# Kernel tuning notes

Hardware: AMD Instinct MI355X
Metric: run time of the kernel (lower is better)

The kernel has to match this reference:

```python
import jax, jax.numpy as jnp
import numpy as np

N = 50000
E = 800000
D = 128          # in_channels == hidden_channels
L = 3            # num_layers
JK = D * L       # jk 'cat' output
H2 = D // 2      # classifier hidden
C = 2            # out classes
EPS = 1e-5


def setup_inputs() -> dict:
    key = jax.random.key(0)
    ks = jax.random.split(key, 16)
    x = jax.random.normal(ks[0], (N, D), dtype=jnp.float32)
    edge_index = jax.random.randint(ks[1], (2, E), 0, N, dtype=jnp.int64)
    s = 0.05
    Wl = jax.random.normal(ks[2], (L, D, D), dtype=jnp.float32) * s   # lin_l (on aggregated), has bias
    bl = jax.random.normal(ks[3], (L, D), dtype=jnp.float32) * s
    Wr = jax.random.normal(ks[4], (L, D, D), dtype=jnp.float32) * s   # lin_r (on root), no bias
    gamma = jnp.ones((L, D), dtype=jnp.float32)
    beta = jnp.zeros((L, D), dtype=jnp.float32)
    rmean = jax.random.normal(ks[5], (L, D), dtype=jnp.float32) * s
    rvar = jax.random.uniform(ks[6], (L, D), dtype=jnp.float32, minval=0.5, maxval=1.5)
    Wc1 = jax.random.normal(ks[7], (JK, H2), dtype=jnp.float32) * s
    bc1 = jax.random.normal(ks[8], (H2,), dtype=jnp.float32) * s
    Wc2 = jax.random.normal(ks[9], (H2, C), dtype=jnp.float32) * s
    bc2 = jax.random.normal(ks[10], (C,), dtype=jnp.float32) * s
    return {"x": x, "edge_index": edge_index, "Wl": Wl, "bl": bl, "Wr": Wr,
            "gamma": gamma, "beta": beta, "rmean": rmean, "rvar": rvar,
            "Wc1": Wc1, "bc1": bc1, "Wc2": Wc2, "bc2": bc2}


def reference(x, edge_index, Wl, bl, Wr, gamma, beta, rmean, rvar, Wc1, bc1, Wc2, bc2):
    src, dst = edge_index[0], edge_index[1]
    # node in-degree (for mean aggregation), clamp to avoid div-by-zero
    deg = jax.ops.segment_sum(jnp.ones((E,), dtype=x.dtype), dst, num_segments=N)
    inv_deg = 1.0 / jnp.maximum(deg, 1.0)  # [N]

    h = x
    layer_outputs = []
    for i in range(L):
        # SAGEConv(mean): out = lin_l(mean_{j in N(i)} h_j) + lin_r(h_i)
        agg = jax.ops.segment_sum(h[src], dst, num_segments=N) * inv_deg[:, None]  # [N, D]
        h = agg @ Wl[i] + bl[i] + h @ Wr[i]
        # BatchNorm (eval: running stats), then ReLU; Dropout is identity in eval
        h = (h - rmean[i]) * jax.lax.rsqrt(rvar[i] + EPS) * gamma[i] + beta[i]
        h = jax.nn.relu(h)
        layer_outputs.append(h)

    jk = jnp.concatenate(layer_outputs, axis=-1)  # [N, L*D]
    z = jax.nn.relu(jk @ Wc1 + bc1)
    logits = z @ Wc2 + bc2  # [N, 2]
    return logits
```

## Files before the change

kernel.cpp:

```cpp
#include <hip/hip_runtime.h>
#include <hip/hip_fp16.h>
#include <cstdint>
#include <cstddef>

#define DD 128
#define JKD 384
#define EPSV 1e-5f
#define BSH 7
#define NBMAX 512
#define PCH 8192
#define PTH 1024
#define BCAP 8192

typedef __attribute__((ext_vector_type(8))) short bf16x8;
typedef __attribute__((ext_vector_type(4))) float f32x4;
#define MFMA(a, b, c) __builtin_amdgcn_mfma_f32_16x16x32_bf16(a, b, c, 0, 0, 0)

__device__ inline unsigned short f2bf_rne(float f) {
  unsigned u = __float_as_uint(f);
  unsigned r = u + 0x7fffu + ((u >> 16) & 1u);
  return (unsigned short)(r >> 16);
}

__device__ inline void split8(const float* s, bf16x8& hi, bf16x8& lo) {
#pragma unroll
  for (int j = 0; j < 8; ++j) {
    float f = s[j];
    unsigned short h = f2bf_rne(f);
    float fh = __uint_as_float((unsigned)h << 16);
    hi[j] = (short)h;
    lo[j] = (short)f2bf_rne(f - fh);
  }
}

__device__ inline void h8_to_f8(uint4 raw, float* out) {
  const __half2* hp = reinterpret_cast<const __half2*>(&raw);
#pragma unroll
  for (int j = 0; j < 4; ++j) {
    float2 f = __half22float2(hp[j]);
    out[2 * j] = f.x;
    out[2 * j + 1] = f.y;
  }
}

__global__ __launch_bounds__(PTH) void bucket_hist(const int* __restrict__ dst,
                                                   int* __restrict__ hist_g, int E) {
  __shared__ int h[NBMAX];
  int t = threadIdx.x;
  for (int i = t; i < NBMAX; i += PTH) h[i] = 0;
  __syncthreads();
  int base = blockIdx.x * PCH;
#pragma unroll
  for (int it = 0; it < PCH / PTH; ++it) {
    int e = base + it * PTH + t;
    if (e < E) {
      int d = __builtin_nontemporal_load(dst + e);
      atomicAdd(&h[d >> BSH], 1);
    }
  }
  __syncthreads();
  for (int i = t; i < NBMAX; i += PTH) hist_g[blockIdx.x * NBMAX + i] = h[i];
}

__global__ __launch_bounds__(512) void bucket_scan(const int* __restrict__ hist_g, int nChunks,
                                                   int* __restrict__ bucket_start,
                                                   int* __restrict__ bucket_cursor,
                                                   int* __restrict__ row_start, int N, int E) {
  __shared__ int wsum[8];
  __shared__ int wpref[8];
  int t = threadIdx.x;
  int lane = t & 63, wid = t >> 6;
  int v = 0;
  for (int c = 0; c < nChunks; ++c) v += hist_g[c * NBMAX + t];
  int sc = v;
#pragma unroll
  for (int off = 1; off < 64; off <<= 1) {
    int u = __shfl_up(sc, off, 64);
    if (lane >= off) sc += u;
  }
  if (lane == 63) wsum[wid] = sc;
  __syncthreads();
  if (t == 0) {
    int a = 0;
#pragma unroll
    for (int w = 0; w < 8; ++w) { wpref[w] = a; a += wsum[w]; }
  }
  __syncthreads();
  int excl = wpref[wid] + sc - v;
  bucket_start[t] = excl;
  bucket_cursor[t] = excl;
  if (t == 0) row_start[N] = E;
}

__global__ __launch_bounds__(PTH) void partition_prep(
    const int* __restrict__ src, const int* __restrict__ dst, int* bucket_cursor,
    unsigned* __restrict__ packed, int E, int nChunks,
    const float* __restrict__ Wl, const float* __restrict__ Wr, bf16x8* __restrict__ wf,
    const float* __restrict__ Wc1, bf16x8* __restrict__ wcf,
    const float* __restrict__ x, unsigned short* __restrict__ x16, int N) {
  __shared__ int h[NBMAX];
  __shared__ int lofs[NBMAX];
  __shared__ int res[NBMAX];
  __shared__ int lcur[NBMAX];
  __shared__ int wsum[4];
  __shared__ int wpref[4];
  __shared__ unsigned stage[PCH];

  if (blockIdx.x < nChunks) {
    int t = threadIdx.x;
    int lane = t & 63;
    int base = blockIdx.x * PCH;
    for (int i = t; i < NBMAX; i += PTH) h[i] = 0;
    __syncthreads();
#pragma unroll
    for (int it = 0; it < PCH / PTH; ++it) {
      int e = base + it * PTH + t;
      if (e < E) {
        int d = __builtin_nontemporal_load(dst + e);
        atomicAdd(&h[d >> BSH], 1);
      }
    }
    __syncthreads();
    int c0 = 0, c1 = 0, s = 0, sc = 0;
    if (t < 256) {
      c0 = h[2 * t];
      c1 = h[2 * t + 1];
      s = c0 + c1;
      sc = s;
#pragma unroll
      for (int off = 1; off < 64; off <<= 1) {
        int u = __shfl_up(sc, off, 64);
        if (lane >= off) sc += u;
      }
      if (lane == 63) wsum[t >> 6] = sc;
    }
    __syncthreads();
    if (t == 0) {
      int a = 0;
#pragma unroll
      for (int w = 0; w < 4; ++w) { wpref[w] = a; a += wsum[w]; }
    }
    __syncthreads();
    if (t < 256) {
      int excl = wpref[t >> 6] + sc - s;
      lofs[2 * t] = excl;
      lofs[2 * t + 1] = excl + c0;
      lcur[2 * t] = excl;
      lcur[2 * t + 1] = excl + c0;
      if (c0 > 0) res[2 * t] = atomicAdd(&bucket_cursor[2 * t], c0);
      if (c1 > 0) res[2 * t + 1] = atomicAdd(&bucket_cursor[2 * t + 1], c1);
    }
    __syncthreads();
#pragma unroll
    for (int it = 0; it < PCH / PTH; ++it) {
      int e = base + it * PTH + t;
      if (e < E) {
        int d = __builtin_nontemporal_load(dst + e);
        int sv = __builtin_nontemporal_load(src + e);
        int pos = atomicAdd(&lcur[d >> BSH], 1);
        stage[pos] = ((unsigned)(d & ((1 << BSH) - 1)) << 16) | (unsigned)(sv & 0xffff);
      }
    }
    __syncthreads();
    int wid = t >> 6;
    for (int b = wid; b < NBMAX; b += PTH / 64) {
      int run = h[b];
      if (run == 0) continue;
      int gbase = res[b], lbase = lofs[b];
      for (int j = lane; j < run; j += 64) packed[gbase + j] = stage[lbase + j];
    }
  } else {
    int sub = threadIdx.x >> 8;
    int t = threadIdx.x & 255;
    int f16blocks = (N * 16 + 255) / 256;
    int vb = (blockIdx.x - nChunks) * 4 + sub;
    if (vb >= 60 + f16blocks) return;
    if (vb < 48) {
      int idx = vb * 256 + t;
      int ln = idx & 63;
      int ksnt = (idx >> 6) & 31;
      int mat = (idx >> 11) & 1;
      int layer = idx >> 12;
      int ks = ksnt >> 3, nt = ksnt & 7;
      int nn = nt * 16 + (ln & 15);
      int k0 = ks * 32 + (ln >> 4) * 8;
      const float* W = (mat ? Wr : Wl) + (size_t)layer * DD * DD;
      float v[8];
#pragma unroll
      for (int j = 0; j < 8; ++j) v[j] = W[(size_t)(k0 + j) * DD + nn];
      bf16x8 hi, lo;
      split8(v, hi, lo);
      size_t base = (size_t)((layer * 2 + mat) * 2) * 2048 + (size_t)ksnt * 64 + ln;
      wf[base] = hi;
      wf[base + 2048] = lo;
    } else if (vb < 60) {
      int idx = (vb - 48) * 256 + t;
      int ln = idx & 63;
      int ksnt = idx >> 6;
      int ks = ksnt >> 2, nt = ksnt & 3;
      int nn = nt * 16 + (ln & 15);
      int k0 = ks * 32 + (ln >> 4) * 8;
      float v[8];
#pragma unroll
      for (int j = 0; j < 8; ++j) v[j] = Wc1[(size_t)(k0 + j) * 64 + nn];
      bf16x8 hi, lo;
      split8(v, hi, lo);
      wcf[idx] = hi;
      wcf[idx + 3072] = lo;
    } else {
      int idx = (vb - 60) * 256 + t;
      int r = idx >> 4, cc = (idx & 15) * 8;
      if (r < N) {
        const float* p = x + (size_t)r * DD + cc;
        float4 a = *reinterpret_cast<const float4*>(p);
        float4 bb = *reinterpret_cast<const float4*>(p + 4);
        __half2 h0 = __floats2half2_rn(a.x, a.y);
        __half2 h1 = __floats2half2_rn(a.z, a.w);
        __half2 h2 = __floats2half2_rn(bb.x, bb.y);
        __half2 h3 = __floats2half2_rn(bb.z, bb.w);
        uint4 o;
        o.x = *reinterpret_cast<unsigned*>(&h0);
        o.y = *reinterpret_cast<unsigned*>(&h1);
        o.z = *reinterpret_cast<unsigned*>(&h2);
        o.w = *reinterpret_cast<unsigned*>(&h3);
        *reinterpret_cast<uint4*>(x16 + (size_t)r * DD + cc) = o;
      }
    }
  }
}

__global__ __launch_bounds__(256) void csr_build(const unsigned* __restrict__ packed,
                                                 const int* __restrict__ bucket_start,
                                                 int* __restrict__ row_start,
                                                 float* __restrict__ inv_deg,
                                                 unsigned short* __restrict__ col, int N) {
  __shared__ int cntA[128];
  __shared__ int lcur[128];
  __shared__ int wsum2[2];
  __shared__ int wpref2[2];
  __shared__ unsigned short stage[BCAP];
  int t = threadIdx.x;
  int b = blockIdx.x;
  int s0 = bucket_start[b], s1 = bucket_start[b + 1];
  int cnt = s1 - s0;
  if (t < 128) cntA[t] = 0;
  __syncthreads();
  for (int i = t; i < cnt; i += 256) {
    unsigned p = packed[s0 + i];
    atomicAdd(&cntA[p >> 16], 1);
  }
  __syncthreads();
  if (t < 128) {
    int lane = t & 63, wid = t >> 6;
    int v = cntA[t];
    int sc = v;
#pragma unroll
    for (int off = 1; off < 64; off <<= 1) {
      int u = __shfl_up(sc, off, 64);
      if (lane >= off) sc += u;
    }
    if (lane == 63) wsum2[wid] = sc;
    __syncthreads();
    if (t == 0) { wpref2[0] = 0; wpref2[1] = wsum2[0]; }
    __syncthreads();
    int excl = wpref2[wid] + sc - v;
    lcur[t] = excl;
    int node = b * 128 + t;
    if (node < N) {
      row_start[node] = s0 + excl;
      inv_deg[node] = 1.0f / fmaxf((float)v, 1.0f);
    }
  } else {
    __syncthreads();
    __syncthreads();
  }
  __syncthreads();
  for (int i = t; i < cnt; i += 256) {
    unsigned p = packed[s0 + i];
    int pos = atomicAdd(&lcur[p >> 16], 1);
    unsigned short us = (unsigned short)(p & 0xffff);
    if (pos < BCAP) stage[pos] = us;
    else col[s0 + pos] = us;
  }
  __syncthreads();
  int lim = min(cnt, BCAP);
  for (int i = t; i < lim; i += 256) col[s0 + i] = stage[i];
}

__global__ __launch_bounds__(256) void agg16_kernel(const unsigned short* __restrict__ h16,
                                                    int ldh,
                                                    const int* __restrict__ row_start,
                                                    const unsigned short* __restrict__ col,
                                                    const float* __restrict__ inv_deg,
                                                    unsigned short* __restrict__ agg16, int n) {
  int wib = threadIdx.x >> 6;
  int lane = threadIdx.x & 63;
  int node = blockIdx.x * 4 + wib;
  if (node >= n) return;
  int beg = row_start[node];
  int end = row_start[node + 1];
  int q = lane >> 4, l15 = lane & 15;
  float acc[8];
#pragma unroll
  for (int k = 0; k < 8; ++k) acc[k] = 0.f;

  for (int j0 = beg; j0 < end; j0 += 16) {
    int cnt = end - j0;
    if (cnt > 16) cnt = 16;
    int cidx = (int)col[j0 + min(l15, cnt - 1)];
    uint4 raw[4];
    bool val[4];
#pragma unroll
    for (int k = 0; k < 4; ++k) {
      int e = k * 4 + q;
      int s = __shfl(cidx, e < cnt ? e : 0);
      val[k] = e < cnt;
      if (val[k]) raw[k] = *reinterpret_cast<const uint4*>(h16 + (size_t)s * ldh + l15 * 8);
    }
#pragma unroll
    for (int k = 0; k < 4; ++k) {
      if (val[k]) {
        float f8[8];
        h8_to_f8(raw[k], f8);
#pragma unroll
        for (int c = 0; c < 8; ++c) acc[c] += f8[c];
      }
    }
  }
#pragma unroll
  for (int m = 16; m <= 32; m <<= 1) {
#pragma unroll
    for (int k = 0; k < 8; ++k) acc[k] += __shfl_xor(acc[k], m);
  }
  if (lane < 16) {
    float w = inv_deg[node];
    __half2 h0 = __floats2half2_rn(acc[0] * w, acc[1] * w);
    __half2 h1 = __floats2half2_rn(acc[2] * w, acc[3] * w);
    __half2 h2 = __floats2half2_rn(acc[4] * w, acc[5] * w);
    __half2 h3 = __floats2half2_rn(acc[6] * w, acc[7] * w);
    uint4 o;
    o.x = *reinterpret_cast<unsigned*>(&h0);
    o.y = *reinterpret_cast<unsigned*>(&h1);
    o.z = *reinterpret_cast<unsigned*>(&h2);
    o.w = *reinterpret_cast<unsigned*>(&h3);
    *reinterpret_cast<uint4*>(agg16 + (size_t)node * DD + l15 * 8) = o;
  }
}

__global__ __launch_bounds__(256) void layer_gemm_mfma(
    const unsigned short* __restrict__ hin16, int ldh,
    const unsigned short* __restrict__ agg16,
    const bf16x8* __restrict__ Blh_g, const bf16x8* __restrict__ Bll_g,
    const bf16x8* __restrict__ Brh_g, const bf16x8* __restrict__ Brl_g,
    const float* __restrict__ bl, const float* __restrict__ gamma,
    const float* __restrict__ beta, const float* __restrict__ rmean,
    const float* __restrict__ rvar, unsigned short* __restrict__ out16, int n) {
  int t = threadIdx.x;
  int w = t >> 6, lane = t & 63;
  int lane16 = lane & 15, quad = lane >> 4;
  int row0 = blockIdx.x * 64;
  int m = row0 + w * 16 + lane16;
  bool valid = m < n;
  size_t mrow = (size_t)(valid ? m : 0);
  const unsigned short* ap = agg16 + mrow * DD + quad * 8;
  const unsigned short* hp = hin16 + mrow * (size_t)ldh + quad * 8;

  bf16x8 Ah[4], Al[4], Hh[4], Hl[4];
#pragma unroll
  for (int ks = 0; ks < 4; ++ks) {
    float a8[8], h8[8];
    if (valid) {
      uint4 ra = *reinterpret_cast<const uint4*>(ap + ks * 32);
      uint4 rh = *reinterpret_cast<const uint4*>(hp + ks * 32);
      h8_to_f8(ra, a8);
      h8_to_f8(rh, h8);
    } else {
#pragma unroll
      for (int j = 0; j < 8; ++j) { a8[j] = 0.f; h8[j] = 0.f; }
    }
    split8(a8, Ah[ks], Al[ks]);
    split8(h8, Hh[ks], Hl[ks]);
  }

  f32x4 acc[8];
#pragma unroll
  for (int nt = 0; nt < 8; ++nt) acc[nt] = (f32x4){0.f, 0.f, 0.f, 0.f};

#pragma unroll
  for (int ks = 0; ks < 4; ++ks) {
    int fb = ks * 8 * 64 + lane;
    bf16x8 B0[8], B1[8];
#pragma unroll
    for (int nt = 0; nt < 8; ++nt) B0[nt] = Blh_g[fb + nt * 64];
#pragma unroll
    for (int nt = 0; nt < 8; ++nt) acc[nt] = MFMA(Ah[ks], B0[nt], acc[nt]);
#pragma unroll
    for (int nt = 0; nt < 8; ++nt) B1[nt] = Bll_g[fb + nt * 64];
#pragma unroll
    for (int nt = 0; nt < 8; ++nt) acc[nt] = MFMA(Al[ks], B0[nt], acc[nt]);
#pragma unroll
    for (int nt = 0; nt < 8; ++nt) acc[nt] = MFMA(Ah[ks], B1[nt], acc[nt]);
#pragma unroll
    for (int nt = 0; nt < 8; ++nt) B0[nt] = Brh_g[fb + nt * 64];
#pragma unroll
    for (int nt = 0; nt < 8; ++nt) acc[nt] = MFMA(Hh[ks], B0[nt], acc[nt]);
#pragma unroll
    for (int nt = 0; nt < 8; ++nt) B1[nt] = Brl_g[fb + nt * 64];
#pragma unroll
    for (int nt = 0; nt < 8; ++nt) acc[nt] = MFMA(Hl[ks], B0[nt], acc[nt]);
#pragma unroll
    for (int nt = 0; nt < 8; ++nt) acc[nt] = MFMA(Hh[ks], B1[nt], acc[nt]);
  }

#pragma unroll
  for (int nt = 0; nt < 8; ++nt) {
    int c = nt * 16 + lane16;
    float sc = gamma[c] * rsqrtf(rvar[c] + EPSV);
    float sh = (bl[c] - rmean[c]) * sc + beta[c];
#pragma unroll
    for (int r = 0; r < 4; ++r) {
      int orow = row0 + w * 16 + quad * 4 + r;
      if (orow < n) {
        float v = fmaxf(fmaf(acc[nt][r], sc, sh), 0.f);
        __half hv = __float2half_rn(v);
        out16[(size_t)orow * JKD + c] = *reinterpret_cast<unsigned short*>(&hv);
      }
    }
  }
}

__global__ __launch_bounds__(256) void gemm2_cls(
    const unsigned short* __restrict__ gsrc, int ldg,
    const unsigned short* __restrict__ agg16,
    const bf16x8* __restrict__ Blh_g, const bf16x8* __restrict__ Bll_g,
    const bf16x8* __restrict__ Brh_g, const bf16x8* __restrict__ Brl_g,
    const float* __restrict__ bl, const float* __restrict__ gamma,
    const float* __restrict__ beta, const float* __restrict__ rmean,
    const float* __restrict__ rvar,
    const unsigned short* __restrict__ jk16, const bf16x8* __restrict__ wcf,
    const float* __restrict__ bc1, const float* __restrict__ Wc2,
    const float* __restrict__ bc2, float* __restrict__ out, int n) {
  __shared__ unsigned short sOut[4][16][136];
  __shared__ float sZ[64][65];
  int t = threadIdx.x;
  int w = t >> 6, lane = t & 63;
  int lane16 = lane & 15, quad = lane >> 4;
  int row0 = blockIdx.x * 64;
  int m = row0 + w * 16 + lane16;
  bool valid = m < n;
  size_t mrow = (size_t)(valid ? m : 0);
  const unsigned short* ap = agg16 + mrow * DD + quad * 8;
  const unsigned short* hp = gsrc + mrow * (size_t)ldg + quad * 8;

  bf16x8 Ah[4], Al[4], Hh[4], Hl[4];
#pragma unroll
  for (int ks = 0; ks < 4; ++ks) {
    float a8[8], h8[8];
    if (valid) {
      uint4 ra = *reinterpret_cast<const uint4*>(ap + ks * 32);
      uint4 rh = *reinterpret_cast<const uint4*>(hp + ks * 32);
      h8_to_f8(ra, a8);
      h8_to_f8(rh, h8);
    } else {
#pragma unroll
      for (int j = 0; j < 8; ++j) { a8[j] = 0.f; h8[j] = 0.f; }
    }
    split8(a8, Ah[ks], Al[ks]);
    split8(h8, Hh[ks], Hl[ks]);
  }

  f32x4 acc[8];
#pragma unroll
  for (int nt = 0; nt < 8; ++nt) acc[nt] = (f32x4){0.f, 0.f, 0.f, 0.f};

#pragma unroll
  for (int ks = 0; ks < 4; ++ks) {
    int fb = ks * 8 * 64 + lane;
    bf16x8 B0[8], B1[8];
#pragma unroll
    for (int nt = 0; nt < 8; ++nt) B0[nt] = Blh_g[fb + nt * 64];
#pragma unroll
    for (int nt = 0; nt < 8; ++nt) acc[nt] = MFMA(Ah[ks], B0[nt], acc[nt]);
#pragma unroll
    for (int nt = 0; nt < 8; ++nt) B1[nt] = Bll_g[fb + nt * 64];
#pragma unroll
    for (int nt = 0; nt < 8; ++nt) acc[nt] = MFMA(Al[ks], B0[nt], acc[nt]);
#pragma unroll
    for (int nt = 0; nt < 8; ++nt) acc[nt] = MFMA(Ah[ks], B1[nt], acc[nt]);
#pragma unroll
    for (int nt = 0; nt < 8; ++nt) B0[nt] = Brh_g[fb + nt * 64];
#pragma unroll
    for (int nt = 0; nt < 8; ++nt) acc[nt] = MFMA(Hh[ks], B0[nt], acc[nt]);
#pragma unroll
    for (int nt = 0; nt < 8; ++nt) B1[nt] = Brl_g[fb + nt * 64];
#pragma unroll
    for (int nt = 0; nt < 8; ++nt) acc[nt] = MFMA(Hl[ks], B0[nt], acc[nt]);
#pragma unroll
    for (int nt = 0; nt < 8; ++nt) acc[nt] = MFMA(Hh[ks], B1[nt], acc[nt]);
  }

#pragma unroll
  for (int nt = 0; nt < 8; ++nt) {
    int c = nt * 16 + lane16;
    float sc = gamma[c] * rsqrtf(rvar[c] + EPSV);
    float sh = (bl[c] - rmean[c]) * sc + beta[c];
#pragma unroll
    for (int r = 0; r < 4; ++r) {
      float v = fmaxf(fmaf(acc[nt][r], sc, sh), 0.f);
      __half hv = __float2half_rn(v);
      sOut[w][quad * 4 + r][c] = *reinterpret_cast<unsigned short*>(&hv);
    }
  }
  __syncthreads();

  const unsigned short* jp = jk16 + mrow * JKD + quad * 8;
  f32x4 cacc[4];
#pragma unroll
  for (int nt = 0; nt < 4; ++nt) cacc[nt] = (f32x4){0.f, 0.f, 0.f, 0.f};

#pragma unroll
  for (int ks = 0; ks < 12; ++ks) {
    float a8[8];
    if (ks < 8) {
      if (valid) {
        uint4 raw = *reinterpret_cast<const uint4*>(jp + ks * 32);
        h8_to_f8(raw, a8);
      } else {
#pragma unroll
        for (int j = 0; j < 8; ++j) a8[j] = 0.f;
      }
    } else {
      uint4 raw = *reinterpret_cast<const uint4*>(&sOut[w][lane16][(ks - 8) * 32 + quad * 8]);
      h8_to_f8(raw, a8);
    }
    bf16x8 Jh, Jl;
    split8(a8, Jh, Jl);
    int fb = ks * 4 * 64 + lane;
    bf16x8 B0[4], B1[4];
#pragma unroll
    for (int nt = 0; nt < 4; ++nt) B0[nt] = wcf[fb + nt * 64];
#pragma unroll
    for (int nt = 0; nt < 4; ++nt) cacc[nt] = MFMA(Jh, B0[nt], cacc[nt]);
#pragma unroll
    for (int nt = 0; nt < 4; ++nt) B1[nt] = wcf[3072 + fb + nt * 64];
#pragma unroll
    for (int nt = 0; nt < 4; ++nt) cacc[nt] = MFMA(Jl, B0[nt], cacc[nt]);
#pragma unroll
    for (int nt = 0; nt < 4; ++nt) cacc[nt] = MFMA(Jh, B1[nt], cacc[nt]);
  }

#pragma unroll
  for (int nt = 0; nt < 4; ++nt) {
    int c = nt * 16 + lane16;
    float b1 = bc1[c];
#pragma unroll
    for (int r = 0; r < 4; ++r)
      sZ[w * 16 + quad * 4 + r][c] = fmaxf(cacc[nt][r] + b1, 0.f);
  }
  __syncthreads();

  if (t < 128) {
    int r = t >> 1, j = t & 1;
    int gr = row0 + r;
    if (gr < n) {
      float s = bc2[j];
#pragma unroll
      for (int c = 0; c < 64; ++c) s = fmaf(sZ[r][c], Wc2[c * 2 + j], s);
      out[(size_t)gr * 2 + j] = s;
    }
  }
}


extern "C" void kernel_launch(void* const* d_in, const int* in_sizes, int n_in,
                              void* d_out, int out_size, void* d_ws, size_t ws_size,
                              hipStream_t stream) {
  const float* x = (const float*)d_in[0];
  const int* ei = (const int*)d_in[1];
  const float* Wl = (const float*)d_in[2];
  const float* bl = (const float*)d_in[3];
  const float* Wr = (const float*)d_in[4];
  const float* gamma = (const float*)d_in[5];
  const float* beta = (const float*)d_in[6];
  const float* rmean = (const float*)d_in[7];
  const float* rvar = (const float*)d_in[8];
  const float* Wc1 = (const float*)d_in[9];
  const float* bc1 = (const float*)d_in[10];
  const float* Wc2 = (const float*)d_in[11];
  const float* bc2 = (const float*)d_in[12];
  float* out = (float*)d_out;

  const int N = in_sizes[0] / DD;
  const int E = in_sizes[1] / 2;
  const int* src = ei;
  const int* dst = ei + E;

  auto align = [](size_t v) { return (v + 255) & ~(size_t)255; };
  char* ws = (char*)d_ws;
  size_t off = 0;
  int* row_start = (int*)(ws + off);  off = align(off + sizeof(int) * (size_t)(N + 1));
  unsigned short* col = (unsigned short*)(ws + off); off = align(off + sizeof(short) * (size_t)E);
  float* inv_deg = (float*)(ws + off); off = align(off + sizeof(float) * (size_t)N);
  unsigned* packed = (unsigned*)(ws + off); off = align(off + sizeof(unsigned) * (size_t)E);
  const int nChunks = (E + PCH - 1) / PCH;
  int* hist_g = (int*)(ws + off);        off = align(off + sizeof(int) * (size_t)nChunks * NBMAX);
  int* bucket_start = (int*)(ws + off);  off = align(off + sizeof(int) * (NBMAX + 1));
  int* bucket_cursor = (int*)(ws + off); off = align(off + sizeof(int) * NBMAX);
  unsigned short* x16 = (unsigned short*)(ws + off);   off = align(off + sizeof(short) * (size_t)N * DD);
  unsigned short* agg16 = (unsigned short*)(ws + off); off = align(off + sizeof(short) * (size_t)N * DD);
  unsigned short* jk16 = (unsigned short*)(ws + off);  off = align(off + sizeof(short) * (size_t)N * JKD);
  bf16x8* wf = (bf16x8*)(ws + off);  off = align(off + (size_t)16 * 3 * 2 * 2 * 2048);
  bf16x8* wcf = (bf16x8*)(ws + off); off = align(off + (size_t)16 * 2 * 3072);

  const int nbuck = (N + 127) >> BSH;
  int f16blocks = (N * 16 + 255) / 256;
  int prepBlocks = (60 + f16blocks + 3) / 4;

  bucket_hist<<<nChunks, PTH, 0, stream>>>(dst, hist_g, E);
  bucket_scan<<<1, 512, 0, stream>>>(hist_g, nChunks, bucket_start, bucket_cursor, row_start, N, E);
  partition_prep<<<nChunks + prepBlocks, PTH, 0, stream>>>(
      src, dst, bucket_cursor, packed, E, nChunks, Wl, Wr, wf, Wc1, wcf, x, x16, N);
  csr_build<<<nbuck, 256, 0, stream>>>(packed, bucket_start, row_start, inv_deg, col, N);

  int nTiles = (N + 63) / 64;
  for (int i = 0; i < 3; ++i) {
    const unsigned short* gsrc = (i == 0) ? x16 : (jk16 + (size_t)(i - 1) * DD);
    int ldg = (i == 0) ? DD : JKD;
    agg16_kernel<<<(N + 3) / 4, 256, 0, stream>>>(gsrc, ldg, row_start, col, inv_deg, agg16, N);
    bf16x8* Wlf = wf + (size_t)(i * 2 + 0) * 2 * 2048;
    bf16x8* Wrf = wf + (size_t)(i * 2 + 1) * 2 * 2048;
    if (i < 2) {
      layer_gemm_mfma<<<nTiles, 256, 0, stream>>>(
          gsrc, ldg, agg16, Wlf, Wlf + 2048, Wrf, Wrf + 2048,
          bl + (size_t)i * DD, gamma + (size_t)i * DD, beta + (size_t)i * DD,
          rmean + (size_t)i * DD, rvar + (size_t)i * DD, jk16 + (size_t)i * DD, N);
    } else {
      gemm2_cls<<<nTiles, 256, 0, stream>>>(
          gsrc, ldg, agg16, Wlf, Wlf + 2048, Wrf, Wrf + 2048,
          bl + (size_t)i * DD, gamma + (size_t)i * DD, beta + (size_t)i * DD,
          rmean + (size_t)i * DD, rvar + (size_t)i * DD,
          jk16, wcf, bc1, Wc2, bc2, out, N);
    }
  }
}
```

Before: 315.0 us.

## Replace histogram/scan with fixed-capacity buckets for CSR partitioning

Drops the bucket histogram and scan kernels and instead assigns each destination bucket a fixed-capacity slot region, initialised by a tiny cursor kernel. The CSR becomes gapped, so per-node row_end is stored and used by aggregation. This removes an extra pass over dst and two launches, but risks overflow if any bucket exceeds the fixed capacity. It also aliases two shared arrays in the classifier kernel to reduce LDS use.

```diff
diff --git a/kernel.cpp b/kernel.cpp
--- a/kernel.cpp
+++ b/kernel.cpp
@@ -8,6 +8,7 @@
 #define EPSV 1e-5f
 #define BSH 7
 #define NBMAX 512
+#define BCAP2 4096
 #define PCH 8192
 #define PTH 1024
 #define BCAP 8192
@@ -43,53 +44,9 @@
   }
 }
 
-__global__ __launch_bounds__(PTH) void bucket_hist(const int* __restrict__ dst,
-                                                   int* __restrict__ hist_g, int E) {
-  __shared__ int h[NBMAX];
+__global__ void init_cursor(int* __restrict__ cursor) {
   int t = threadIdx.x;
-  for (int i = t; i < NBMAX; i += PTH) h[i] = 0;
-  __syncthreads();
-  int base = blockIdx.x * PCH;
-#pragma unroll
-  for (int it = 0; it < PCH / PTH; ++it) {
-    int e = base + it * PTH + t;
-    if (e < E) {
-      int d = __builtin_nontemporal_load(dst + e);
-      atomicAdd(&h[d >> BSH], 1);
-    }
-  }
-  __syncthreads();
-  for (int i = t; i < NBMAX; i += PTH) hist_g[blockIdx.x * NBMAX + i] = h[i];
-}
-
-__global__ __launch_bounds__(512) void bucket_scan(const int* __restrict__ hist_g, int nChunks,
-                                                   int* __restrict__ bucket_start,
-                                                   int* __restrict__ bucket_cursor,
-                                                   int* __restrict__ row_start, int N, int E) {
-  __shared__ int wsum[8];
-  __shared__ int wpref[8];
-  int t = threadIdx.x;
-  int lane = t & 63, wid = t >> 6;
-  int v = 0;
-  for (int c = 0; c < nChunks; ++c) v += hist_g[c * NBMAX + t];
-  int sc = v;
-#pragma unroll
-  for (int off = 1; off < 64; off <<= 1) {
-    int u = __shfl_up(sc, off, 64);
-    if (lane >= off) sc += u;
-  }
-  if (lane == 63) wsum[wid] = sc;
-  __syncthreads();
-  if (t == 0) {
-    int a = 0;
-#pragma unroll
-    for (int w = 0; w < 8; ++w) { wpref[w] = a; a += wsum[w]; }
-  }
-  __syncthreads();
-  int excl = wpref[wid] + sc - v;
-  bucket_start[t] = excl;
-  bucket_cursor[t] = excl;
-  if (t == 0) row_start[N] = E;
+  if (t < NBMAX) cursor[t] = t * BCAP2;
 }
 
 __global__ __launch_bounds__(PTH) void partition_prep(
@@ -230,8 +187,9 @@
 }
 
 __global__ __launch_bounds__(256) void csr_build(const unsigned* __restrict__ packed,
-                                                 const int* __restrict__ bucket_start,
+                                                 const int* __restrict__ bucket_cursor,
                                                  int* __restrict__ row_start,
+                                                 int* __restrict__ row_end,
                                                  float* __restrict__ inv_deg,
                                                  unsigned short* __restrict__ col, int N) {
   __shared__ int cntA[128];
@@ -241,8 +199,8 @@
   __shared__ unsigned short stage[BCAP];
   int t = threadIdx.x;
   int b = blockIdx.x;
-  int s0 = bucket_start[b], s1 = bucket_start[b + 1];
-  int cnt = s1 - s0;
+  int s0 = b * BCAP2;
+  int cnt = bucket_cursor[b] - s0;
   if (t < 128) cntA[t] = 0;
   __syncthreads();
   for (int i = t; i < cnt; i += 256) {
@@ -268,6 +226,7 @@
     int node = b * 128 + t;
     if (node < N) {
       row_start[node] = s0 + excl;
+      row_end[node] = s0 + excl + v;
       inv_deg[node] = 1.0f / fmaxf((float)v, 1.0f);
     }
   } else {
@@ -290,6 +249,7 @@
 __global__ __launch_bounds__(256) void agg16_kernel(const unsigned short* __restrict__ h16,
                                                     int ldh,
                                                     const int* __restrict__ row_start,
+                                                    const int* __restrict__ row_end,
                                                     const unsigned short* __restrict__ col,
                                                     const float* __restrict__ inv_deg,
                                                     unsigned short* __restrict__ agg16, int n) {
@@ -298,7 +258,7 @@
   int node = blockIdx.x * 4 + wib;
   if (node >= n) return;
   int beg = row_start[node];
-  int end = row_start[node + 1];
+  int end = row_end[node];
   int q = lane >> 4, l15 = lane & 15;
   float acc[8];
 #pragma unroll
@@ -440,8 +400,9 @@
     const unsigned short* __restrict__ jk16, const bf16x8* __restrict__ wcf,
     const float* __restrict__ bc1, const float* __restrict__ Wc2,
     const float* __restrict__ bc2, float* __restrict__ out, int n) {
-  __shared__ unsigned short sOut[4][16][136];
-  __shared__ float sZ[64][65];
+  __shared__ __align__(16) unsigned char smem[4 * 16 * 136 * 2];
+  unsigned short (*sOut)[16][136] = reinterpret_cast<unsigned short(*)[16][136]>(smem);
+  float (*sZ)[65] = reinterpret_cast<float(*)[65]>(smem);
   int t = threadIdx.x;
   int w = t >> 6, lane = t & 63;
   int lane16 = lane & 15, quad = lane >> 4;
@@ -548,6 +509,7 @@
 #pragma unroll
     for (int nt = 0; nt < 4; ++nt) cacc[nt] = MFMA(Jh, B1[nt], cacc[nt]);
   }
+  __syncthreads();
 
 #pragma unroll
   for (int nt = 0; nt < 4; ++nt) {
@@ -598,13 +560,11 @@
   auto align = [](size_t v) { return (v + 255) & ~(size_t)255; };
   char* ws = (char*)d_ws;
   size_t off = 0;
-  int* row_start = (int*)(ws + off);  off = align(off + sizeof(int) * (size_t)(N + 1));
-  unsigned short* col = (unsigned short*)(ws + off); off = align(off + sizeof(short) * (size_t)E);
+  int* row_start = (int*)(ws + off);  off = align(off + sizeof(int) * (size_t)N);
+  int* row_end = (int*)(ws + off);    off = align(off + sizeof(int) * (size_t)N);
+  unsigned short* col = (unsigned short*)(ws + off); off = align(off + sizeof(short) * (size_t)NBMAX * BCAP2);
   float* inv_deg = (float*)(ws + off); off = align(off + sizeof(float) * (size_t)N);
-  unsigned* packed = (unsigned*)(ws + off); off = align(off + sizeof(unsigned) * (size_t)E);
-  const int nChunks = (E + PCH - 1) / PCH;
-  int* hist_g = (int*)(ws + off);        off = align(off + sizeof(int) * (size_t)nChunks * NBMAX);
-  int* bucket_start = (int*)(ws + off);  off = align(off + sizeof(int) * (NBMAX + 1));
+  unsigned* packed = (unsigned*)(ws + off); off = align(off + sizeof(unsigned) * (size_t)NBMAX * BCAP2);
   int* bucket_cursor = (int*)(ws + off); off = align(off + sizeof(int) * NBMAX);
   unsigned short* x16 = (unsigned short*)(ws + off);   off = align(off + sizeof(short) * (size_t)N * DD);
   unsigned short* agg16 = (unsigned short*)(ws + off); off = align(off + sizeof(short) * (size_t)N * DD);
@@ -613,20 +573,20 @@
   bf16x8* wcf = (bf16x8*)(ws + off); off = align(off + (size_t)16 * 2 * 3072);
 
   const int nbuck = (N + 127) >> BSH;
+  const int nChunks = (E + PCH - 1) / PCH;
   int f16blocks = (N * 16 + 255) / 256;
   int prepBlocks = (60 + f16blocks + 3) / 4;
 
-  bucket_hist<<<nChunks, PTH, 0, stream>>>(dst, hist_g, E);
-  bucket_scan<<<1, 512, 0, stream>>>(hist_g, nChunks, bucket_start, bucket_cursor, row_start, N, E);
+  init_cursor<<<1, NBMAX, 0, stream>>>(bucket_cursor);
   partition_prep<<<nChunks + prepBlocks, PTH, 0, stream>>>(
       src, dst, bucket_cursor, packed, E, nChunks, Wl, Wr, wf, Wc1, wcf, x, x16, N);
-  csr_build<<<nbuck, 256, 0, stream>>>(packed, bucket_start, row_start, inv_deg, col, N);
+  csr_build<<<nbuck, 256, 0, stream>>>(packed, bucket_cursor, row_start, row_end, inv_deg, col, N);
 
   int nTiles = (N + 63) / 64;
   for (int i = 0; i < 3; ++i) {
     const unsigned short* gsrc = (i == 0) ? x16 : (jk16 + (size_t)(i - 1) * DD);
     int ldg = (i == 0) ? DD : JKD;
-    agg16_kernel<<<(N + 3) / 4, 256, 0, stream>>>(gsrc, ldg, row_start, col, inv_deg, agg16, N);
+    agg16_kernel<<<(N + 3) / 4, 256, 0, stream>>>(gsrc, ldg, row_start, row_end, col, inv_deg, agg16, N);
     bf16x8* Wlf = wf + (size_t)(i * 2 + 0) * 2 * 2048;
     bf16x8* Wrf = wf + (size_t)(i * 2 + 1) * 2 * 2048;
     if (i < 2) {
```

Result: faster. 307.0 us (-2.5%).
